# Performance work log

Measured on AMD Instinct MI355X. Metric: run time of the kernel, lower is better.

## Reference

```python
import jax, jax.numpy as jnp
import numpy as np

B, N, D, H, L = 8, 1025, 1024, 8, 2   # N = maxlen + 1
NUM_BUCKETS = 64
EPS = 1e-8


def layernorm(x):
    mu = jnp.mean(x, axis=-1, keepdims=True)
    var = jnp.mean((x - mu) ** 2, axis=-1, keepdims=True)
    return (x - mu) / jnp.sqrt(var + EPS)


def rmsnorm(x):
    return x * jax.lax.rsqrt(jnp.mean(x * x, axis=-1, keepdims=True) + EPS)


def rel_attn_bias(action_ts, ts_w, pos_w):
    # positional part: pos_w[j - i + N - 1]  (equivalent to the pad/repeat trick)
    idx = jnp.arange(N)[None, :] - jnp.arange(N)[:, None] + (N - 1)  # [N,N] in [0,2N-2]
    rel_pos = pos_w[idx][None]  # [1,N,N]
    # time part: bucketize ext[i+1] - ext[j], ext = cat(ts, ts[:, N-1:N])
    ext = jnp.concatenate([action_ts, action_ts[:, N - 1:N]], axis=1)  # [B,N+1]
    diff = ext[:, 1:, None] - ext[:, None, :-1]  # [B,N,N]
    bucket = (jnp.log(jnp.clip(jnp.abs(diff), 1, None).astype(jnp.float32)) / 0.301).astype(jnp.int32)
    bucket = jnp.clip(bucket, 0, NUM_BUCKETS)
    rel_ts = ts_w[bucket]  # [B,N,N]
    return rel_pos + rel_ts


def hstu_block(x, mask, bias, qkvu, out_w, out_b, fc1_w, fc1_b, fc2_w, fc2_b):
    hd = D // H
    xn = layernorm(x)
    qkvu_act = jax.nn.silu(xn @ qkvu)  # [B,N,4D]
    q, k, v, u = jnp.split(qkvu_act, 4, axis=-1)
    q = q.reshape(B, N, H, hd)
    k = k.reshape(B, N, H, hd)
    v = v.reshape(B, N, H, hd)
    scores = jnp.einsum('bihd,bjhd->bhij', q, k) + bias[:, None]  # [B,H,N,N]
    attn = jax.nn.silu(scores) / N * mask[:, None]
    av = jnp.einsum('bhij,bjhd->bihd', attn, v).reshape(B, N, D)
    attn_out = (u * layernorm(av)) @ out_w + out_b
    h = x + attn_out
    # SwiGLU FFN (mult=2) with RMSNorm pre-norm and residual
    vg = rmsnorm(h) @ fc1_w + fc1_b  # [B,N,4D]
    vv, g = jnp.split(vg, 2, axis=-1)
    y = (jax.nn.silu(g) * vv) @ fc2_w + fc2_b
    return h + y


def setup_inputs() -> dict:
    key = jax.random.key(0)
    ks = jax.random.split(key, 12)
    std = 0.02
    seqs = jax.random.normal(ks[0], (B, N, D), jnp.float32)
    mask = jnp.tril(jnp.ones((N, N), jnp.float32))[None].repeat(B, axis=0)
    action_ts = jnp.sort(jax.random.randint(ks[1], (B, N), 0, 1000000000).astype(jnp.int64), axis=1)
    return {
        'seqs': seqs,
        'mask': mask,
        'action_ts': action_ts,
        'qkvu': jax.random.normal(ks[2], (L, D, 4 * D), jnp.float32) * std,
        'out_w': jax.random.normal(ks[3], (L, D, D), jnp.float32) * std,
        'out_b': jnp.zeros((L, D), jnp.float32),
        'ts_w': jax.random.normal(ks[4], (L, NUM_BUCKETS + 1), jnp.float32) * std,
        'pos_w': jax.random.normal(ks[5], (L, 2 * N - 1), jnp.float32) * std,
        'fc1_w': jax.random.normal(ks[6], (L, D, 4 * D), jnp.float32) * std,
        'fc1_b': jnp.zeros((L, 4 * D), jnp.float32),
        'fc2_w': jax.random.normal(ks[7], (L, 2 * D, D), jnp.float32) * std,
        'fc2_b': jnp.zeros((L, D), jnp.float32),
    }


def reference(seqs, mask, action_ts, qkvu, out_w, out_b, ts_w, pos_w, fc1_w, fc1_b, fc2_w, fc2_b):
    h = seqs
    for l in range(L):
        bias = rel_attn_bias(action_ts, ts_w[l], pos_w[l])
        h = hstu_block(h, mask, bias, qkvu[l], out_w[l], out_b[l],
                       fc1_w[l], fc1_b[l], fc2_w[l], fc2_b[l])
    return h
```

## Files before the change

kernel.cpp:

```cpp
#include <hip/hip_runtime.h>
#include <hip/hip_bf16.h>
#include <math.h>

#define BB 8
#define SEQN 1025
#define DD 1024
#define HH 8
#define HD 128
#define LL 2
#define MROWS (BB*SEQN)
#define NBUCKET 64

using short8 = __attribute__((ext_vector_type(8))) short;
using f32x4  = __attribute__((ext_vector_type(4))) float;
using f32x16 = __attribute__((ext_vector_type(16))) float;

__device__ __forceinline__ float silu_f(float x) { return x / (1.f + expf(-x)); }

__device__ __forceinline__ float bf2f(ushort u) {
  union { uint i; float f; } x; x.i = ((uint)u) << 16; return x.f;
}
__device__ __forceinline__ ushort f2bf(float f) {
  __hip_bfloat16 b = __float2bfloat16(f);
  return *reinterpret_cast<ushort*>(&b);
}
__device__ __forceinline__ void gll16(const void* g, void* l) {
  __builtin_amdgcn_global_load_lds((const __attribute__((address_space(1))) void*)g,
                                   (__attribute__((address_space(3))) void*)l, 16, 0, 0);
}
__device__ __forceinline__ uint pkbf(float lo, float hi) {
  uint r;
  asm("v_cvt_pk_bf16_f32 %0, %1, %2" : "=v"(r) : "v"(lo), "v"(hi));
  return r;
}
__device__ __forceinline__ f32x16 z16() {
  f32x16 v;
#pragma unroll
  for (int i = 0; i < 16; ++i) v[i] = 0.f;
  return v;
}

__global__ __launch_bounds__(256) void copy_kernel(const float* __restrict__ in,
                                                   float* __restrict__ out, int n4) {
  int idx = blockIdx.x * blockDim.x + threadIdx.x;
  int stride = gridDim.x * blockDim.x;
  const float4* i4 = (const float4*)in;
  float4* o4 = (float4*)out;
  for (int i = idx; i < n4; i += stride) o4[i] = i4[i];
}

__global__ __launch_bounds__(256) void wtrans(const float* __restrict__ W,
                                              ushort* __restrict__ Wt, int K, int N) {
  __shared__ float tile[32][33];
  int tid = threadIdx.x;
  int tx = tid & 31, ty = tid >> 5;
  int n0 = blockIdx.x * 32, k0 = blockIdx.y * 32;
#pragma unroll
  for (int r = 0; r < 32; r += 8)
    tile[ty + r][tx] = W[(size_t)(k0 + ty + r) * N + n0 + tx];
  __syncthreads();
#pragma unroll
  for (int r = 0; r < 32; r += 8)
    Wt[(size_t)(n0 + ty + r) * K + k0 + tx] = f2bf(tile[tx][ty + r]);
}

__global__ __launch_bounds__(256) void bias_kernel(const int* __restrict__ ts,
    const float* __restrict__ ts_w, const float* __restrict__ pos_w,
    ushort* __restrict__ biasT)
{
  int i = blockIdx.x * 256 + threadIdx.x;
  int j = blockIdx.y;
  int b = blockIdx.z;
  if (i >= SEQN) return;
  int ip1 = i + 1; if (ip1 > SEQN - 1) ip1 = SEQN - 1;
  long long t1 = (long long)ts[b * SEQN + ip1];
  long long t0 = (long long)ts[b * SEQN + j];
  long long d = t1 - t0;
  if (d < 0) d = -d;
  if (d < 1) d = 1;
  int bucket = (int)(logf((float)d) / 0.301f);
  if (bucket < 0) bucket = 0;
  if (bucket > NBUCKET) bucket = NBUCKET;
  biasT[((size_t)(b * SEQN + j)) * SEQN + i] = f2bf(pos_w[j - i + SEQN - 1] + ts_w[bucket]);
}

__global__ __launch_bounds__(256) void ln_kernel(const float* __restrict__ in,
                                                 ushort* __restrict__ out) {
  int row = blockIdx.x;
  int tid = threadIdx.x;
  const float* x = in + (size_t)row * DD;
  float4 v = *(const float4*)&x[tid * 4];
  float s = v.x + v.y + v.z + v.w;
  float ss = v.x*v.x + v.y*v.y + v.z*v.z + v.w*v.w;
#pragma unroll
  for (int off = 32; off >= 1; off >>= 1) { s += __shfl_xor(s, off); ss += __shfl_xor(ss, off); }
  __shared__ float red0[4], red1[4];
  if ((tid & 63) == 0) { red0[tid >> 6] = s; red1[tid >> 6] = ss; }
  __syncthreads();
  s = red0[0] + red0[1] + red0[2] + red0[3];
  ss = red1[0] + red1[1] + red1[2] + red1[3];
  float mu = s * (1.f / DD);
  float var = fmaxf(ss * (1.f / DD) - mu * mu, 0.f);
  float inv = 1.f / sqrtf(var + 1e-8f);
  ushort4 o;
  o.x = f2bf((v.x - mu) * inv); o.y = f2bf((v.y - mu) * inv);
  o.z = f2bf((v.z - mu) * inv); o.w = f2bf((v.w - mu) * inv);
  *(ushort4*)&out[(size_t)row * DD + tid * 4] = o;
}

__global__ __launch_bounds__(256) void rms_kernel(const float* __restrict__ in,
                                                  ushort* __restrict__ out) {
  int row = blockIdx.x;
  int tid = threadIdx.x;
  const float* x = in + (size_t)row * DD;
  float4 v = *(const float4*)&x[tid * 4];
  float ss = v.x*v.x + v.y*v.y + v.z*v.z + v.w*v.w;
#pragma unroll
  for (int off = 32; off >= 1; off >>= 1) ss += __shfl_xor(ss, off);
  __shared__ float red1[4];
  if ((tid & 63) == 0) red1[tid >> 6] = ss;
  __syncthreads();
  ss = red1[0] + red1[1] + red1[2] + red1[3];
  float inv = 1.f / sqrtf(ss * (1.f / DD) + 1e-8f);
  ushort4 o;
  o.x = f2bf(v.x * inv); o.y = f2bf(v.y * inv);
  o.z = f2bf(v.z * inv); o.w = f2bf(v.w * inv);
  *(ushort4*)&out[(size_t)row * DD + tid * 4] = o;
}

__global__ __launch_bounds__(256) void uln_kernel(const float* __restrict__ av,
    const ushort* __restrict__ act, ushort* __restrict__ out) {
  int row = blockIdx.x;
  int tid = threadIdx.x;
  const float* x = av + (size_t)row * DD;
  float4 v = *(const float4*)&x[tid * 4];
  float s = v.x + v.y + v.z + v.w;
  float ss = v.x*v.x + v.y*v.y + v.z*v.z + v.w*v.w;
#pragma unroll
  for (int off = 32; off >= 1; off >>= 1) { s += __shfl_xor(s, off); ss += __shfl_xor(ss, off); }
  __shared__ float red0[4], red1[4];
  if ((tid & 63) == 0) { red0[tid >> 6] = s; red1[tid >> 6] = ss; }
  __syncthreads();
  s = red0[0] + red0[1] + red0[2] + red0[3];
  ss = red1[0] + red1[1] + red1[2] + red1[3];
  float mu = s * (1.f / DD);
  float var = fmaxf(ss * (1.f / DD) - mu * mu, 0.f);
  float inv = 1.f / sqrtf(var + 1e-8f);
  ushort4 uu = *(const ushort4*)&act[(size_t)row * 4096 + 3072 + tid * 4];
  ushort4 o;
  o.x = f2bf(bf2f(uu.x) * (v.x - mu) * inv);
  o.y = f2bf(bf2f(uu.y) * (v.y - mu) * inv);
  o.z = f2bf(bf2f(uu.z) * (v.z - mu) * inv);
  o.w = f2bf(bf2f(uu.w) * (v.w - mu) * inv);
  *(ushort4*)&out[(size_t)row * DD + tid * 4] = o;
}

__global__ __launch_bounds__(256) void mgemm1(const ushort* __restrict__ A,
    const ushort* __restrict__ Bt, const float* __restrict__ bvec,
    float* __restrict__ Cout, int M, int Nn, int K)
{
  __shared__ ushort As[3][4096];
  __shared__ ushort Bs[3][4096];
  const int tid  = threadIdx.x;
  const int lane = tid & 63, wave = tid >> 6;
  const int wm = wave >> 1, wn = wave & 1;
  const int lrow = lane & 15, lk = lane >> 4;
  const int bm = blockIdx.y * 128, bn = blockIdx.x * 128;

  const ushort* Aga[2]; const ushort* Bga[2];
  ushort* Ada[2]; ushort* Bda[2];
#pragma unroll
  for (int i = 0; i < 2; ++i) {
    int c = tid + 256 * i;
    int row = c >> 2, s = c & 3;
    int sc = s ^ ((row >> 1) & 3);
    Aga[i] = A  + (size_t)(bm + row) * K + sc * 8;
    Bga[i] = Bt + (size_t)(bn + row) * K + sc * 8;
    Ada[i] = &As[0][c * 8];
    Bda[i] = &Bs[0][c * 8];
  }

  int aoff[4], boff[4];
#pragma unroll
  for (int m = 0; m < 4; ++m)
    aoff[m] = (wm * 64 + m * 16 + lrow) * 32 + ((lk ^ ((lrow >> 1) & 3)) * 8);
#pragma unroll
  for (int n = 0; n < 4; ++n)
    boff[n] = (wn * 64 + n * 16 + lrow) * 32 + ((lk ^ ((lrow >> 1) & 3)) * 8);

  f32x4 acc[4][4];
#pragma unroll
  for (int m = 0; m < 4; ++m)
#pragma unroll
    for (int n = 0; n < 4; ++n) acc[m][n] = (f32x4){0.f, 0.f, 0.f, 0.f};

  const int nk = K >> 5;
#pragma unroll
  for (int t = 0; t < 2; ++t) {
#pragma unroll
    for (int i = 0; i < 2; ++i) {
      gll16(Aga[i] + (t << 5), Ada[i] + t * 4096);
      gll16(Bga[i] + (t << 5), Bda[i] + t * 4096);
    }
  }
  int cur = 0, nxt2 = 2;
  for (int kt = 0; kt < nk; ++kt) {
    if (kt + 1 < nk) {
      asm volatile("s_waitcnt vmcnt(4)" ::: "memory");
    } else {
      asm volatile("s_waitcnt vmcnt(0)" ::: "memory");
    }
    __builtin_amdgcn_s_barrier();
    __builtin_amdgcn_sched_barrier(0);
    if (kt + 2 < nk) {
      const int ko = (kt + 2) << 5;
      const int bo = nxt2 * 4096;
#pragma unroll
      for (int i = 0; i < 2; ++i) {
        gll16(Aga[i] + ko, Ada[i] + bo);
        gll16(Bga[i] + ko, Bda[i] + bo);
      }
    }
    __builtin_amdgcn_s_setprio(1);
    {
      short8 af[4], bfr[4];
      const int co = cur * 4096;
#pragma unroll
      for (int m = 0; m < 4; ++m) af[m]  = *(const short8*)&As[0][co + aoff[m]];
#pragma unroll
      for (int n = 0; n < 4; ++n) bfr[n] = *(const short8*)&Bs[0][co + boff[n]];
#pragma unroll
      for (int m = 0; m < 4; ++m)
#pragma unroll
        for (int n = 0; n < 4; ++n)
          acc[m][n] = __builtin_amdgcn_mfma_f32_16x16x32_bf16(af[m], bfr[n], acc[m][n], 0, 0, 0);
    }
    __builtin_amdgcn_s_setprio(0);
    __builtin_amdgcn_sched_barrier(0);
    cur = (cur == 2) ? 0 : cur + 1;
    nxt2 = (nxt2 == 2) ? 0 : nxt2 + 1;
  }

  const int colbase = bn + wn * 64 + lrow;
  const int rowbase = bm + wm * 64 + lk * 4;
#pragma unroll
  for (int m = 0; m < 4; ++m) {
    int row0 = rowbase + m * 16;
#pragma unroll
    for (int n = 0; n < 4; ++n) {
      int col = colbase + n * 16;
      float bv = bvec[col];
#pragma unroll
      for (int r = 0; r < 4; ++r) {
        int row = row0 + r;
        if (row < M) {
          float* p = Cout + (size_t)row * Nn + col;
          *p += acc[m][n][r] + bv;
        }
      }
    }
  }
}

template<int MODE>
__global__ __launch_bounds__(512, 2) void mgemm8(const ushort* __restrict__ A,
    const ushort* __restrict__ Bt, const float* __restrict__ bvec,
    void* __restrict__ Cout, int M, int Nn, int K)
{
  __shared__ ushort LS[65536];
  const int tid = threadIdx.x;
  const int lane = tid & 63, wave = tid >> 6;
  const int wm = wave >> 2, wn = wave & 3;
  const int lrow = lane & 15, lk = lane >> 4;
  const int bm = blockIdx.y * 256;

  const ushort* srcA[2]; const ushort* srcB[2];
  int ldsA[2], ldsB[2];
#pragma unroll
  for (int i = 0; i < 2; ++i) {
    int c = tid + 512 * i, row = c >> 2, s = c & 3;
    int sw = (s ^ ((row >> 1) & 3)) * 8;
    srcA[i] = A + (size_t)(bm + row) * K + sw;
    ldsA[i] = c * 8;
    int gr;
    if (MODE == 3) {
      gr = blockIdx.x * 128 + (row >> 5) * 16 + ((row >> 4) & 1) * 2048 + (row & 15);
    } else {
      gr = blockIdx.x * 256 + row;
    }
    srcB[i] = Bt + (size_t)gr * K + sw;
    ldsB[i] = c * 8;
  }
  int aoff[8], boff[4];
#pragma unroll
  for (int m = 0; m < 8; ++m)
    aoff[m] = (wm * 128 + m * 16 + lrow) * 32 + ((lk ^ ((lrow >> 1) & 3)) * 8);
#pragma unroll
  for (int n = 0; n < 4; ++n)
    boff[n] = (wn * 64 + n * 16 + lrow) * 32 + ((lk ^ ((lrow >> 1) & 3)) * 8);

  f32x4 acc[8][4];
#pragma unroll
  for (int m = 0; m < 8; ++m)
#pragma unroll
    for (int n = 0; n < 4; ++n) acc[m][n] = (f32x4){0.f, 0.f, 0.f, 0.f};

  const int NT = K >> 6;

#define STG_A(T, H, B)                                                        \
  { _Pragma("unroll")                                                         \
    for (int i = 0; i < 2; ++i)                                               \
      gll16(srcA[i] + ((T) << 6) + ((H) << 5),                                \
            (void*)&LS[((B) * 2 + (H)) * 8192 + ldsA[i]]); }
#define STG_B(T, H, B)                                                        \
  { _Pragma("unroll")                                                         \
    for (int i = 0; i < 2; ++i)                                               \
      gll16(srcB[i] + ((T) << 6) + ((H) << 5),                                \
            (void*)&LS[32768 + ((B) * 2 + (H)) * 8192 + ldsB[i]]); }

#define TILE4(T, B)                                                           \
  {                                                                           \
    const int t_ = (T);                                                       \
                                                                      \
    { int ts = (t_ + 1 < NT) ? t_ + 1 : NT - 1; STG_A(ts, 1, (B) ^ 1); }      \
    asm volatile("s_waitcnt vmcnt(10)" ::: "memory");                         \
    __builtin_amdgcn_s_barrier();                                             \
    __builtin_amdgcn_sched_barrier(0);                                        \
    short8 bfr[4];                                                            \
    _Pragma("unroll")                                                         \
    for (int n = 0; n < 4; ++n)                                               \
      bfr[n] = *(const short8*)&LS[32768 + ((B) * 2 + 0) * 8192 + boff[n]];   \
    {                                                                         \
      short8 af[4];                                                           \
      _Pragma("unroll")                                                       \
      for (int mi = 0; mi < 4; ++mi)                                          \
        af[mi] = *(const short8*)&LS[((B) * 2 + 0) * 8192 + aoff[mi]];        \
      __builtin_amdgcn_s_setprio(1);                                          \
      _Pragma("unroll")                                                       \
      for (int mi = 0; mi < 4; ++mi)                                          \
        _Pragma("unroll")                                                     \
        for (int n = 0; n < 4; ++n)                                           \
          acc[mi][n] = __builtin_amdgcn_mfma_f32_16x16x32_bf16(af[mi], bfr[n], acc[mi][n], 0, 0, 0); \
      __builtin_amdgcn_s_setprio(0);                                          \
    }                                                                         \
                                                                      \
    { int ts = (t_ + 1 < NT) ? t_ + 1 : NT - 1; STG_B(ts, 1, (B) ^ 1); }      \
    {                                                                         \
      short8 af[4];                                                           \
      _Pragma("unroll")                                                       \
      for (int mi = 0; mi < 4; ++mi)                                          \
        af[mi] = *(const short8*)&LS[((B) * 2 + 0) * 8192 + aoff[4 + mi]];    \
      __builtin_amdgcn_s_setprio(1);                                          \
      _Pragma("unroll")                                                       \
      for (int mi = 0; mi < 4; ++mi)                                          \
        _Pragma("unroll")                                                     \
        for (int n = 0; n < 4; ++n)                                           \
          acc[4 + mi][n] = __builtin_amdgcn_mfma_f32_16x16x32_bf16(af[mi], bfr[n], acc[4 + mi][n], 0, 0, 0); \
      __builtin_amdgcn_s_setprio(0);                                          \
    }                                                                         \
    __builtin_amdgcn_sched_barrier(0);                                        \
    __builtin_amdgcn_s_barrier();              \
                                                                      \
    { int ts = (t_ + 2 < NT) ? t_ + 2 : NT - 1; STG_A(ts, 0, (B)); }          \
    asm volatile("s_waitcnt vmcnt(10)" ::: "memory");                         \
    __builtin_amdgcn_s_barrier();                                             \
    __builtin_amdgcn_sched_barrier(0);                                        \
    _Pragma("unroll")                                                         \
    for (int n = 0; n < 4; ++n)                                               \
      bfr[n] = *(const short8*)&LS[32768 + ((B) * 2 + 1) * 8192 + boff[n]];   \
    {                                                                         \
      short8 af[4];                                                           \
      _Pragma("unroll")                                                       \
      for (int mi = 0; mi < 4; ++mi)                                          \
        af[mi] = *(const short8*)&LS[((B) * 2 + 1) * 8192 + aoff[mi]];        \
      __builtin_amdgcn_s_setprio(1);                                          \
      _Pragma("unroll")                                                       \
      for (int mi = 0; mi < 4; ++mi)                                          \
        _Pragma("unroll")                                                     \
        for (int n = 0; n < 4; ++n)                                           \
          acc[mi][n] = __builtin_amdgcn_mfma_f32_16x16x32_bf16(af[mi], bfr[n], acc[mi][n], 0, 0, 0); \
      __builtin_amdgcn_s_setprio(0);                                          \
    }                                                                         \
                                                                      \
    { int ts = (t_ + 2 < NT) ? t_ + 2 : NT - 1; STG_B(ts, 0, (B)); }          \
    {                                                                         \
      short8 af[4];                                                           \
      _Pragma("unroll")                                                       \
      for (int mi = 0; mi < 4; ++mi)                                          \
        af[mi] = *(const short8*)&LS[((B) * 2 + 1) * 8192 + aoff[4 + mi]];    \
      __builtin_amdgcn_s_setprio(1);                                          \
      _Pragma("unroll")                                                       \
      for (int mi = 0; mi < 4; ++mi)                                          \
        _Pragma("unroll")                                                     \
        for (int n = 0; n < 4; ++n)                                           \
          acc[4 + mi][n] = __builtin_amdgcn_mfma_f32_16x16x32_bf16(af[mi], bfr[n], acc[4 + mi][n], 0, 0, 0); \
      __builtin_amdgcn_s_setprio(0);                                          \
    }                                                                         \
    __builtin_amdgcn_sched_barrier(0);                                        \
    __builtin_amdgcn_s_barrier();              \
  }

  STG_A(0, 0, 0); STG_B(0, 0, 0); STG_A(0, 1, 0); STG_B(0, 1, 0);
  STG_A(1, 0, 1); STG_B(1, 0, 1);
  for (int tt = 0; tt < NT; tt += 2) {
    TILE4(tt, 0);
    TILE4(tt + 1, 1);
  }
#undef TILE4
#undef STG_A
#undef STG_B

  const int rowb0 = bm + wm * 128 + lk * 4;
  if (MODE == 0) {
    const int colb0 = blockIdx.x * 256 + wn * 64 + lrow;
    __hip_bfloat16* Cb = (__hip_bfloat16*)Cout;
#pragma unroll
    for (int m = 0; m < 8; ++m) {
      int row0 = rowb0 + m * 16;
#pragma unroll
      for (int n = 0; n < 4; ++n) {
        int col = colb0 + n * 16;
#pragma unroll
        for (int r = 0; r < 4; ++r) {
          int row = row0 + r;
          if (row < M)
            Cb[(size_t)row * Nn + col] = __float2bfloat16(silu_f(acc[m][n][r]));
        }
      }
    }
  } else {
    __hip_bfloat16* Cb = (__hip_bfloat16*)Cout;
#pragma unroll
    for (int q = 0; q < 2; ++q) {
      int vcol = blockIdx.x * 128 + (2 * wn + q) * 16 + lrow;
      float bvv = bvec[vcol];
      float bvg = bvec[vcol + 2048];
#pragma unroll
      for (int m = 0; m < 8; ++m) {
        int row0 = rowb0 + m * 16;
#pragma unroll
        for (int r = 0; r < 4; ++r) {
          int row = row0 + r;
          if (row < M) {
            float v = acc[m][2 * q][r] + bvv;
            float g = acc[m][2 * q + 1][r] + bvg;
            Cb[(size_t)row * 2048 + vcol] = __float2bfloat16(silu_f(g) * v);
          }
        }
      }
    }
  }
}

__global__ __launch_bounds__(256) void attn_kernel(const ushort* __restrict__ act,
    const ushort* __restrict__ biasT, float* __restrict__ av)
{
  __shared__ __align__(16) char KL[8192];
  __shared__ __align__(16) char VL[8320];
  const int tid = threadIdx.x;
  const int l = tid & 63, w = tid >> 6;
  const int qi = (int)(gridDim.x - 1 - blockIdx.x);
  const int i0 = qi * 128;
  const int h = blockIdx.y, b = blockIdx.z;
  const int lo31 = l & 31, hi = l >> 5;

  const int jlim = (i0 + 128 < SEQN) ? i0 + 128 : SEQN;
  const int nt = (jlim + 31) >> 5;

  const int gi_q = i0 + w * 32 + lo31;
  const int gi_qc = gi_q < SEQN ? gi_q : SEQN - 1;
  const size_t actB = (size_t)b * SEQN;
  const ushort* qrow = act + (actB + gi_qc) * 4096 + h * HD;
  short8 qreg[8];
#pragma unroll
  for (int dc = 0; dc < 8; ++dc)
    qreg[dc] = *(const short8*)(qrow + dc * 16 + hi * 8);

  f32x16 acc[4];
#pragma unroll
  for (int dt = 0; dt < 4; ++dt) acc[dt] = z16();

  const int id0 = tid, id1 = tid + 256;
  const int j_0 = id0 >> 4, c8_0 = (id0 & 15) * 8;
  const int j_1 = id1 >> 4, c8_1 = (id1 & 15) * 8;
  char* kw0 = KL + j_0 * 256 + (((id0 & 15) ^ (j_0 & 15)) << 4);
  char* kw1 = KL + j_1 * 256 + (((id1 & 15) ^ (j_1 & 15)) << 4);
  char* vw0 = VL + ((id0 & 15) >> 1) * 1040 + j_0 * 32 + (id0 & 1) * 16;
  char* vw1 = VL + ((id1 & 15) >> 1) * 1040 + j_1 * 32 + (id1 & 1) * 16;
  const uint vbase = (uint)(size_t)(__attribute__((address_space(3))) char*)
      (VL + ((l >> 4) & 1) * 1040 + hi * 256 + (l & 15) * 8);

  short8 kr0, kr1, vr0, vr1;
  {
    const ushort* p0 = act + (actB + j_0) * 4096 + 1024 + h * HD + c8_0;
    const ushort* p1 = act + (actB + j_1) * 4096 + 1024 + h * HD + c8_1;
    kr0 = *(const short8*)p0; vr0 = *(const short8*)(p0 + 1024);
    kr1 = *(const short8*)p1; vr1 = *(const short8*)(p1 + 1024);
  }
  const float invN = 1.f / (float)SEQN;
  const int gi0w = i0 + w * 32;

  for (int t = 0; t < nt; ++t) {
    const int j0 = t * 32;
    __syncthreads();
    *(short8*)kw0 = kr0; *(short8*)kw1 = kr1;
    *(short8*)vw0 = vr0; *(short8*)vw1 = vr1;
    __syncthreads();
    if (t + 1 < nt) {
      const ushort* p0 = act + (actB + j0 + 32 + j_0) * 4096 + 1024 + h * HD + c8_0;
      const ushort* p1 = act + (actB + j0 + 32 + j_1) * 4096 + 1024 + h * HD + c8_1;
      kr0 = *(const short8*)p0; vr0 = *(const short8*)(p0 + 1024);
      kr1 = *(const short8*)p1; vr1 = *(const short8*)(p1 + 1024);
    }
    if (j0 <= gi0w + 31 && gi0w < SEQN) {
      float bv[16];
#pragma unroll
      for (int r = 0; r < 16; ++r) {
        int j = (r & 3) + 8 * (r >> 2) + 4 * hi;
        int gj = j0 + j;
        int gjc = gj < SEQN ? gj : SEQN - 1;
        bv[r] = bf2f(biasT[(actB + gjc) * SEQN + gi_qc]);
      }
      f32x16 st = z16();
#pragma unroll
      for (int dc = 0; dc < 8; ++dc) {
        short8 kf = *(const short8*)(KL + lo31 * 256 + ((((dc << 1) + hi) ^ (lo31 & 15)) << 4));
        st = __builtin_amdgcn_mfma_f32_32x32x16_bf16(kf, qreg[dc], st, 0, 0, 0);
      }
      float p[16];
#pragma unroll
      for (int r = 0; r < 16; ++r) {
        int j = (r & 3) + 8 * (r >> 2) + 4 * hi;
        int gj = j0 + j;
        float s = st[r] + bv[r];
        float pw = s * __builtin_amdgcn_rcpf(1.f + __expf(-s)) * invN;
        p[r] = ((gj <= gi_q) && (gi_q < SEQN)) ? pw : 0.f;
      }
      short8 paf[2];
#pragma unroll
      for (int g = 0; g < 2; ++g) {
        uint w0 = pkbf(p[g * 8 + 0], p[g * 8 + 1]);
        uint w2 = pkbf(p[g * 8 + 4], p[g * 8 + 5]);
        uint w1 = pkbf(p[g * 8 + 2], p[g * 8 + 3]);
        uint w3 = pkbf(p[g * 8 + 6], p[g * 8 + 7]);
        asm volatile("v_permlane32_swap_b32 %0, %1" : "+v"(w0), "+v"(w2));
        asm volatile("v_permlane32_swap_b32 %0, %1" : "+v"(w1), "+v"(w3));
        union UF { uint u[4]; short8 s; } uf;
        uf.u[0] = w0; uf.u[1] = w1; uf.u[2] = w2; uf.u[3] = w3;
        paf[g] = uf.s;
      }
      uint64_t v00, v01, v02, v03, v10, v11, v12, v13, v20, v21, v22, v23, v30, v31, v32, v33;
      asm volatile(
        "ds_read_b64_tr_b16 %0, %16 offset:0\n\t"
        "ds_read_b64_tr_b16 %1, %16 offset:128\n\t"
        "ds_read_b64_tr_b16 %2, %16 offset:512\n\t"
        "ds_read_b64_tr_b16 %3, %16 offset:640\n\t"
        "ds_read_b64_tr_b16 %4, %16 offset:2080\n\t"
        "ds_read_b64_tr_b16 %5, %16 offset:2208\n\t"
        "ds_read_b64_tr_b16 %6, %16 offset:2592\n\t"
        "ds_read_b64_tr_b16 %7, %16 offset:2720\n\t"
        "ds_read_b64_tr_b16 %8, %16 offset:4160\n\t"
        "ds_read_b64_tr_b16 %9, %16 offset:4288\n\t"
        "ds_read_b64_tr_b16 %10, %16 offset:4672\n\t"
        "ds_read_b64_tr_b16 %11, %16 offset:4800\n\t"
        "ds_read_b64_tr_b16 %12, %16 offset:6240\n\t"
        "ds_read_b64_tr_b16 %13, %16 offset:6368\n\t"
        "ds_read_b64_tr_b16 %14, %16 offset:6752\n\t"
        "ds_read_b64_tr_b16 %15, %16 offset:6880\n\t"
        "s_waitcnt lgkmcnt(0)"
        : "=v"(v00), "=v"(v01), "=v"(v02), "=v"(v03),
          "=v"(v10), "=v"(v11), "=v"(v12), "=v"(v13),
          "=v"(v20), "=v"(v21), "=v"(v22), "=v"(v23),
          "=v"(v30), "=v"(v31), "=v"(v32), "=v"(v33)
        : "v"(vbase) : "memory");
      union UV { uint64_t q[2]; short8 s; };
      { UV uv; uv.q[0] = v00; uv.q[1] = v01;
        acc[0] = __builtin_amdgcn_mfma_f32_32x32x16_bf16(paf[0], uv.s, acc[0], 0, 0, 0); }
      { UV uv; uv.q[0] = v02; uv.q[1] = v03;
        acc[0] = __builtin_amdgcn_mfma_f32_32x32x16_bf16(paf[1], uv.s, acc[0], 0, 0, 0); }
      { UV uv; uv.q[0] = v10; uv.q[1] = v11;
        acc[1] = __builtin_amdgcn_mfma_f32_32x32x16_bf16(paf[0], uv.s, acc[1], 0, 0, 0); }
      { UV uv; uv.q[0] = v12; uv.q[1] = v13;
        acc[1] = __builtin_amdgcn_mfma_f32_32x32x16_bf16(paf[1], uv.s, acc[1], 0, 0, 0); }
      { UV uv; uv.q[0] = v20; uv.q[1] = v21;
        acc[2] = __builtin_amdgcn_mfma_f32_32x32x16_bf16(paf[0], uv.s, acc[2], 0, 0, 0); }
      { UV uv; uv.q[0] = v22; uv.q[1] = v23;
        acc[2] = __builtin_amdgcn_mfma_f32_32x32x16_bf16(paf[1], uv.s, acc[2], 0, 0, 0); }
      { UV uv; uv.q[0] = v30; uv.q[1] = v31;
        acc[3] = __builtin_amdgcn_mfma_f32_32x32x16_bf16(paf[0], uv.s, acc[3], 0, 0, 0); }
      { UV uv; uv.q[0] = v32; uv.q[1] = v33;
        acc[3] = __builtin_amdgcn_mfma_f32_32x32x16_bf16(paf[1], uv.s, acc[3], 0, 0, 0); }
    }
  }
#pragma unroll
  for (int dt = 0; dt < 4; ++dt) {
#pragma unroll
    for (int r = 0; r < 16; ++r) {
      int q = (r & 3) + 8 * (r >> 2) + 4 * hi;
      int gi = i0 + w * 32 + q;
      if (gi < SEQN)
        av[(actB + gi) * DD + h * HD + dt * 32 + lo31] = acc[dt][r];
    }
  }
}

extern "C" void kernel_launch(void* const* d_in, const int* in_sizes, int n_in,
                              void* d_out, int out_size, void* d_ws, size_t ws_size,
                              hipStream_t stream) {
  const float* seqs  = (const float*)d_in[0];
  const int*   ts    = (const int*)d_in[2];
  const float* qkvuW = (const float*)d_in[3];
  const float* outW  = (const float*)d_in[4];
  const float* outB  = (const float*)d_in[5];
  const float* tsW   = (const float*)d_in[6];
  const float* posW  = (const float*)d_in[7];
  const float* fc1W  = (const float*)d_in[8];
  const float* fc1B  = (const float*)d_in[9];
  const float* fc2W  = (const float*)d_in[10];
  const float* fc2B  = (const float*)d_in[11];
  float* h = (float*)d_out;
  char* ws = (char*)d_ws;

  ushort* xn    = (ushort*)(ws);
  ushort* act   = (ushort*)(ws + 17301504);
  ushort* gated = (ushort*)(ws + 84475904);
  ushort* biasT = (ushort*)(ws + 118554624);
  float*  av    = (float*) (ws + 152174624);
  ushort* wq    = (ushort*)(ws + 185761824);
  ushort* wo    = (ushort*)(ws + 194150432);
  ushort* wf1   = (ushort*)(ws + 196247584);
  ushort* wf2   = (ushort*)(ws + 204636192);

  copy_kernel<<<2048, 256, 0, stream>>>(seqs, h, MROWS * DD / 4);

  for (int l = 0; l < LL; l++) {
    wtrans<<<dim3(128, 32), 256, 0, stream>>>(qkvuW + (size_t)l * DD * 4096, wq, DD, 4096);
    wtrans<<<dim3(32, 32),  256, 0, stream>>>(outW  + (size_t)l * DD * DD,   wo, DD, DD);
    wtrans<<<dim3(128, 32), 256, 0, stream>>>(fc1W  + (size_t)l * DD * 4096, wf1, DD, 4096);
    wtrans<<<dim3(32, 64),  256, 0, stream>>>(fc2W  + (size_t)l * 2048 * DD, wf2, 2048, DD);

    bias_kernel<<<dim3(5, SEQN, BB), 256, 0, stream>>>(
        ts, tsW + l * (NBUCKET + 1), posW + l * (2 * SEQN - 1), biasT);

    ln_kernel<<<MROWS, 256, 0, stream>>>(h, xn);
    mgemm8<0><<<dim3(16, 33), 512, 0, stream>>>(xn, wq, nullptr, act, MROWS, 4096, DD);
    attn_kernel<<<dim3(9, HH, BB), 256, 0, stream>>>(act, biasT, av);
    uln_kernel<<<MROWS, 256, 0, stream>>>(av, act, xn);
    mgemm1<<<dim3(8, 65), 256, 0, stream>>>(xn, wo, outB + l * DD, h, MROWS, DD, DD);
    rms_kernel<<<MROWS, 256, 0, stream>>>(h, xn);
    mgemm8<3><<<dim3(16, 33), 512, 0, stream>>>(xn, wf1, fc1B + (size_t)l * 4096, gated, MROWS, 2048, DD);
    mgemm1<<<dim3(8, 65), 256, 0, stream>>>(gated, wf2, fc2B + l * DD, h, MROWS, DD, 2048);
  }
}
```

Baseline: 1.085 ms.

## Fuse initial copy into layernorm, store attention output as bf16, double-buffer K/V

Drops the standalone copy of the input into the output buffer and has the first layer's layernorm kernel write the residual copy while it normalizes. The attention kernel now writes its output as bf16 instead of fp32, halving the write and the readback in the following layernorm. The attention K/V shared-memory tiles are double-buffered so the leading __syncthreads per tile can be removed. The trade-offs are extra LDS per block, which may reduce occupancy, and bf16 rounding of the attention output before the layernorm.

```diff
diff --git a/kernel.cpp b/kernel.cpp
--- a/kernel.cpp
+++ b/kernel.cpp
@@ -38,15 +38,6 @@
 #pragma unroll
   for (int i = 0; i < 16; ++i) v[i] = 0.f;
   return v;
-}
-
-__global__ __launch_bounds__(256) void copy_kernel(const float* __restrict__ in,
-                                                   float* __restrict__ out, int n4) {
-  int idx = blockIdx.x * blockDim.x + threadIdx.x;
-  int stride = gridDim.x * blockDim.x;
-  const float4* i4 = (const float4*)in;
-  float4* o4 = (float4*)out;
-  for (int i = idx; i < n4; i += stride) o4[i] = i4[i];
 }
 
 __global__ __launch_bounds__(256) void wtrans(const float* __restrict__ W,
@@ -84,6 +75,31 @@
   biasT[((size_t)(b * SEQN + j)) * SEQN + i] = f2bf(pos_w[j - i + SEQN - 1] + ts_w[bucket]);
 }
 
+__global__ __launch_bounds__(256) void lnh_kernel(const float* __restrict__ in,
+    float* __restrict__ hout, ushort* __restrict__ out) {
+  int row = blockIdx.x;
+  int tid = threadIdx.x;
+  const float* x = in + (size_t)row * DD;
+  float4 v = *(const float4*)&x[tid * 4];
+  float s = v.x + v.y + v.z + v.w;
+  float ss = v.x*v.x + v.y*v.y + v.z*v.z + v.w*v.w;
+#pragma unroll
+  for (int off = 32; off >= 1; off >>= 1) { s += __shfl_xor(s, off); ss += __shfl_xor(ss, off); }
+  __shared__ float red0[4], red1[4];
+  if ((tid & 63) == 0) { red0[tid >> 6] = s; red1[tid >> 6] = ss; }
+  __syncthreads();
+  s = red0[0] + red0[1] + red0[2] + red0[3];
+  ss = red1[0] + red1[1] + red1[2] + red1[3];
+  float mu = s * (1.f / DD);
+  float var = fmaxf(ss * (1.f / DD) - mu * mu, 0.f);
+  float inv = 1.f / sqrtf(var + 1e-8f);
+  *(float4*)&hout[(size_t)row * DD + tid * 4] = v;
+  ushort4 o;
+  o.x = f2bf((v.x - mu) * inv); o.y = f2bf((v.y - mu) * inv);
+  o.z = f2bf((v.z - mu) * inv); o.w = f2bf((v.w - mu) * inv);
+  *(ushort4*)&out[(size_t)row * DD + tid * 4] = o;
+}
+
 __global__ __launch_bounds__(256) void ln_kernel(const float* __restrict__ in,
                                                  ushort* __restrict__ out) {
   int row = blockIdx.x;
@@ -128,12 +144,13 @@
   *(ushort4*)&out[(size_t)row * DD + tid * 4] = o;
 }
 
-__global__ __launch_bounds__(256) void uln_kernel(const float* __restrict__ av,
+__global__ __launch_bounds__(256) void uln_kernel(const ushort* __restrict__ av,
     const ushort* __restrict__ act, ushort* __restrict__ out) {
   int row = blockIdx.x;
   int tid = threadIdx.x;
-  const float* x = av + (size_t)row * DD;
-  float4 v = *(const float4*)&x[tid * 4];
+  ushort4 ub = *(const ushort4*)&av[(size_t)row * DD + tid * 4];
+  float4 v;
+  v.x = bf2f(ub.x); v.y = bf2f(ub.y); v.z = bf2f(ub.z); v.w = bf2f(ub.w);
   float s = v.x + v.y + v.z + v.w;
   float ss = v.x*v.x + v.y*v.y + v.z*v.z + v.w*v.w;
 #pragma unroll
@@ -321,7 +338,6 @@
 #define TILE4(T, B)                                                           \
   {                                                                           \
     const int t_ = (T);                                                       \
-                                                                      \
     { int ts = (t_ + 1 < NT) ? t_ + 1 : NT - 1; STG_A(ts, 1, (B) ^ 1); }      \
     asm volatile("s_waitcnt vmcnt(10)" ::: "memory");                         \
     __builtin_amdgcn_s_barrier();                                             \
@@ -343,7 +359,6 @@
           acc[mi][n] = __builtin_amdgcn_mfma_f32_16x16x32_bf16(af[mi], bfr[n], acc[mi][n], 0, 0, 0); \
       __builtin_amdgcn_s_setprio(0);                                          \
     }                                                                         \
-                                                                      \
     { int ts = (t_ + 1 < NT) ? t_ + 1 : NT - 1; STG_B(ts, 1, (B) ^ 1); }      \
     {                                                                         \
       short8 af[4];                                                           \
@@ -359,8 +374,7 @@
       __builtin_amdgcn_s_setprio(0);                                          \
     }                                                                         \
     __builtin_amdgcn_sched_barrier(0);                                        \
-    __builtin_amdgcn_s_barrier();              \
-                                                                      \
+    __builtin_amdgcn_s_barrier();                                             \
     { int ts = (t_ + 2 < NT) ? t_ + 2 : NT - 1; STG_A(ts, 0, (B)); }          \
     asm volatile("s_waitcnt vmcnt(10)" ::: "memory");                         \
     __builtin_amdgcn_s_barrier();                                             \
@@ -381,7 +395,6 @@
           acc[mi][n] = __builtin_amdgcn_mfma_f32_16x16x32_bf16(af[mi], bfr[n], acc[mi][n], 0, 0, 0); \
       __builtin_amdgcn_s_setprio(0);                                          \
     }                                                                         \
-                                                                      \
     { int ts = (t_ + 2 < NT) ? t_ + 2 : NT - 1; STG_B(ts, 0, (B)); }          \
     {                                                                         \
       short8 af[4];                                                           \
@@ -397,7 +410,7 @@
       __builtin_amdgcn_s_setprio(0);                                          \
     }                                                                         \
     __builtin_amdgcn_sched_barrier(0);                                        \
-    __builtin_amdgcn_s_barrier();              \
+    __builtin_amdgcn_s_barrier();                                             \
   }
 
   STG_A(0, 0, 0); STG_B(0, 0, 0); STG_A(0, 1, 0); STG_B(0, 1, 0);
@@ -453,10 +466,10 @@
 }
 
 __global__ __launch_bounds__(256) void attn_kernel(const ushort* __restrict__ act,
-    const ushort* __restrict__ biasT, float* __restrict__ av)
+    const ushort* __restrict__ biasT, ushort* __restrict__ av)
 {
-  __shared__ __align__(16) char KL[8192];
-  __shared__ __align__(16) char VL[8320];
+  __shared__ __align__(16) char KL[16384];
+  __shared__ __align__(16) char VL[16640];
   const int tid = threadIdx.x;
   const int l = tid & 63, w = tid >> 6;
   const int qi = (int)(gridDim.x - 1 - blockIdx.x);
@@ -487,7 +500,7 @@
   char* kw1 = KL + j_1 * 256 + (((id1 & 15) ^ (j_1 & 15)) << 4);
   char* vw0 = VL + ((id0 & 15) >> 1) * 1040 + j_0 * 32 + (id0 & 1) * 16;
   char* vw1 = VL + ((id1 & 15) >> 1) * 1040 + j_1 * 32 + (id1 & 1) * 16;
-  const uint vbase = (uint)(size_t)(__attribute__((address_space(3))) char*)
+  const uint vbase0 = (uint)(size_t)(__attribute__((address_space(3))) char*)
       (VL + ((l >> 4) & 1) * 1040 + hi * 256 + (l & 15) * 8);
 
   short8 kr0, kr1, vr0, vr1;
@@ -502,9 +515,10 @@
 
   for (int t = 0; t < nt; ++t) {
     const int j0 = t * 32;
-    __syncthreads();
-    *(short8*)kw0 = kr0; *(short8*)kw1 = kr1;
-    *(short8*)vw0 = vr0; *(short8*)vw1 = vr1;
+    const int kb = (t & 1) * 8192;
+    const int vb = (t & 1) * 8320;
+    *(short8*)(kw0 + kb) = kr0; *(short8*)(kw1 + kb) = kr1;
+    *(short8*)(vw0 + vb) = vr0; *(short8*)(vw1 + vb) = vr1;
     __syncthreads();
     if (t + 1 < nt) {
       const ushort* p0 = act + (actB + j0 + 32 + j_0) * 4096 + 1024 + h * HD + c8_0;
@@ -524,7 +538,7 @@
       f32x16 st = z16();
 #pragma unroll
       for (int dc = 0; dc < 8; ++dc) {
-        short8 kf = *(const short8*)(KL + lo31 * 256 + ((((dc << 1) + hi) ^ (lo31 & 15)) << 4));
+        short8 kf = *(const short8*)(KL + kb + lo31 * 256 + ((((dc << 1) + hi) ^ (lo31 & 15)) << 4));
         st = __builtin_amdgcn_mfma_f32_32x32x16_bf16(kf, qreg[dc], st, 0, 0, 0);
       }
       float p[16];
@@ -549,6 +563,7 @@
         uf.u[0] = w0; uf.u[1] = w1; uf.u[2] = w2; uf.u[3] = w3;
         paf[g] = uf.s;
       }
+      const uint vbase = vbase0 + vb;
       uint64_t v00, v01, v02, v03, v10, v11, v12, v13, v20, v21, v22, v23, v30, v31, v32, v33;
       asm volatile(
         "ds_read_b64_tr_b16 %0, %16 offset:0\n\t"
@@ -599,7 +614,7 @@
       int q = (r & 3) + 8 * (r >> 2) + 4 * hi;
       int gi = i0 + w * 32 + q;
       if (gi < SEQN)
-        av[(actB + gi) * DD + h * HD + dt * 32 + lo31] = acc[dt][r];
+        av[(actB + gi) * DD + h * HD + dt * 32 + lo31] = f2bf(acc[dt][r]);
     }
   }
 }
@@ -625,13 +640,11 @@
   ushort* act   = (ushort*)(ws + 17301504);
   ushort* gated = (ushort*)(ws + 84475904);
   ushort* biasT = (ushort*)(ws + 118554624);
-  float*  av    = (float*) (ws + 152174624);
+  ushort* av    = (ushort*)(ws + 152174624);
   ushort* wq    = (ushort*)(ws + 185761824);
   ushort* wo    = (ushort*)(ws + 194150432);
   ushort* wf1   = (ushort*)(ws + 196247584);
   ushort* wf2   = (ushort*)(ws + 204636192);
-
-  copy_kernel<<<2048, 256, 0, stream>>>(seqs, h, MROWS * DD / 4);
 
   for (int l = 0; l < LL; l++) {
     wtrans<<<dim3(128, 32), 256, 0, stream>>>(qkvuW + (size_t)l * DD * 4096, wq, DD, 4096);
@@ -642,7 +655,10 @@
     bias_kernel<<<dim3(5, SEQN, BB), 256, 0, stream>>>(
         ts, tsW + l * (NBUCKET + 1), posW + l * (2 * SEQN - 1), biasT);
 
-    ln_kernel<<<MROWS, 256, 0, stream>>>(h, xn);
+    if (l == 0)
+      lnh_kernel<<<MROWS, 256, 0, stream>>>(seqs, h, xn);
+    else
+      ln_kernel<<<MROWS, 256, 0, stream>>>(h, xn);
     mgemm8<0><<<dim3(16, 33), 512, 0, stream>>>(xn, wq, nullptr, act, MROWS, 4096, DD);
     attn_kernel<<<dim3(9, HH, BB), 256, 0, stream>>>(act, biasT, av);
     uln_kernel<<<MROWS, 256, 0, stream>>>(av, act, xn);
```

New measurement: 1.072 ms. Within noise of the previous version (-1.2%).
